# Kernel tuning notes

Measured on AMD Instinct MI355X. Metric: run time of the kernel, lower is better.

The kernel has to match this reference:

```python
import jax, jax.numpy as jnp
import numpy as np

K_MAX_X = 16
K_MAX_T = 16


def _k_actual(N, k_max):
    # low-mode indices [0..k_max] ++ [N-k_max..N-1], mapped to signed frequencies
    idx = np.concatenate([np.arange(k_max + 1), np.arange(N - k_max, N)]).astype(np.float32)
    return np.where(idx <= (N - 1) // 2, idx, idx - N)


def _phase(N, k_max, sign):
    # separable 1D truncated DFT factor: exp(sign*2*pi*i*k*n/N)/sqrt(N), shape [modes, N]
    k = _k_actual(N, k_max)
    n = np.arange(N, dtype=np.float32)
    ang = sign * 2.0 * np.pi * k[:, None] * n[None, :] / N
    return jnp.asarray((np.exp(1j * ang) / np.sqrt(N)).astype(np.complex64))


def setup_inputs() -> dict:
    key = jax.random.key(0)
    k1, k2, k3 = jax.random.split(key, 3)
    B, C_in, C_out, H, W = 16, 64, 64, 128, 128
    modes = 2 * K_MAX_X + 1  # 33
    scale = 1.0 / (C_in * C_out)
    x = jax.random.normal(k1, (B, C_in, H, W), dtype=jnp.float32)
    wr = scale * jax.random.uniform(k2, (C_in, C_out, modes, modes), dtype=jnp.float32)
    wi = scale * jax.random.uniform(k3, (C_in, C_out, modes, modes), dtype=jnp.float32)
    return {"x": x, "weights_real": wr, "weights_imag": wi}


def reference(x, weights_real, weights_imag):
    B, C, H, W = x.shape
    Px_f = _phase(H, K_MAX_X, -1.0)  # [mx, H]
    Pt_f = _phase(W, K_MAX_T, -1.0)  # [mt, W]
    Px_i = _phase(H, K_MAX_X, +1.0)
    Pt_i = _phase(W, K_MAX_T, +1.0)
    xc = x.astype(jnp.complex64)
    # truncated 2D DFT (separable): X[b,c,i,j]
    X = jnp.einsum('bcnm,in,jm->bcij', xc, Px_f, Pt_f)
    R = (weights_real + 1j * weights_imag).astype(jnp.complex64)
    out_kept = jnp.einsum('bcij,coij->boij', X, R)
    # truncated inverse DFT back to grid
    out = jnp.einsum('boij,in,jm->bonm', out_kept, Px_i, Pt_i)
    return jnp.real(out)
```

## Files before the change

kernel.cpp:

```cpp
#include <hip/hip_runtime.h>


#define NB   16
#define NC   64
#define NO   64
#define NH   128
#define NW   128
#define NM   33
#define WMODE (NM*NM)
#define MPAD  1092
#define NIMG 1024

typedef __attribute__((ext_vector_type(8))) short s8v;
typedef __attribute__((ext_vector_type(4))) float f4v;

__device__ inline unsigned short f2bf(float f) {
  union { float f; unsigned u; } v; v.f = f;
  unsigned r = (v.u + 0x7FFFu + ((v.u >> 16) & 1u)) >> 16;
  return (unsigned short)r;
}

__device__ inline s8v pack8(float4 a, float4 b) {
  s8v r;
  r[0] = (short)f2bf(a.x); r[1] = (short)f2bf(a.y);
  r[2] = (short)f2bf(a.z); r[3] = (short)f2bf(a.w);
  r[4] = (short)f2bf(b.x); r[5] = (short)f2bf(b.y);
  r[6] = (short)f2bf(b.z); r[7] = (short)f2bf(b.w);
  return r;
}

__device__ inline uint2 pack4(f4v a) {
  uint2 p;
  p.x = (unsigned)f2bf(a[0]) | ((unsigned)f2bf(a[1]) << 16);
  p.y = (unsigned)f2bf(a[2]) | ((unsigned)f2bf(a[3]) << 16);
  return p;
}

__device__ inline unsigned short phase_bf(int f, int x) {
  if (f >= 66) return 0;
  int g = (f < 33) ? f : f - 33;
  int fr = (g <= 16) ? g : g + 95;
  int ph = (fr * x) & 127;
  float ang = (float)ph * 0.04908738521234052f;
  float v = ((f < 33) ? cosf(ang) : sinf(ang)) * 0.08838834764831845f;
  return f2bf(v);
}

__global__ __launch_bounds__(256) void spc_tables(short* __restrict__ T1,
                                                  short* __restrict__ T2,
                                                  short* __restrict__ T3,
                                                  short* __restrict__ T4) {
  int tid = blockIdx.x * 256 + threadIdx.x;
  if (tid >= 49152) return;
  int f, x; short* dst;
  if (tid < 10240) {
    int e = tid & 7, l = (tid >> 3) & 63, q = tid >> 9;
    int ks = q / 5, jt = q - 5 * ks;
    f = jt * 16 + (l & 15); x = ks * 32 + (l >> 4) * 8 + e; dst = T1 + tid;
  } else if (tid < 20480) {
    int u = tid - 10240;
    int e = u & 7, l = (u >> 3) & 63, q = u >> 9;
    int it = q >> 2, ks = q & 3;
    f = it * 16 + (l & 15); x = ks * 32 + (l >> 4) * 8 + e; dst = T2 + u;
  } else if (tid < 36864) {
    int u = tid - 20480;
    int e = u & 7, l = (u >> 3) & 63, q = u >> 9;
    int cs = q >> 4, ks = (q >> 3) & 1, mt = q & 7;
    int j = ks * 32 + (l >> 4) * 8 + e;
    f = (j < 33) ? cs * 33 + j : 66;
    x = mt * 16 + (l & 15); dst = T3 + u;
  } else {
    int u = tid - 36864;
    int e = u & 7, l = (u >> 3) & 63, q = u >> 9;
    int nt = q / 3, ks = q - 3 * nt;
    int i2 = ks * 32 + (l >> 4) * 8 + e;
    if (i2 < 48) f = (i2 < 33) ? i2 : 66;
    else         f = (i2 - 48 < 33) ? 33 + (i2 - 48) : 66;
    x = nt * 16 + (l & 15); dst = T4 + u;
  }
  *dst = (short)phase_bf(f, x);
}

__global__ __launch_bounds__(256) void spc_fwd_mfma(const float* __restrict__ x,
                                                    const s8v* __restrict__ T1,
                                                    const s8v* __restrict__ T2,
                                                    unsigned* __restrict__ X2u) {
  __shared__ short Wt[80 * 128];
  __shared__ float Gs[80 * 84];
  const int t = threadIdx.x;
  const int l = t & 63;
  const int w = t >> 6;
  const int lr = l & 15;
  const int lg = l >> 4;
  const int img = blockIdx.x;
  const float* xp = x + (size_t)img * (NH * NW);

  for (int nn = 0; nn < 2; ++nn) {
    const int nt = 2 * w + nn;
    const float* xrow = xp + (nt * 16 + lr) * NW + lg * 8;
    s8v a[4];
#pragma unroll
    for (int ks = 0; ks < 4; ++ks) {
      float4 f0 = *reinterpret_cast<const float4*>(xrow + ks * 32);
      float4 f1 = *reinterpret_cast<const float4*>(xrow + ks * 32 + 4);
      a[ks] = pack8(f0, f1);
    }
#pragma unroll
    for (int jt = 0; jt < 5; ++jt) {
      f4v acc = {0.f, 0.f, 0.f, 0.f};
#pragma unroll
      for (int ks = 0; ks < 4; ++ks) {
        s8v b = T1[(ks * 5 + jt) * 64 + l];
        acc = __builtin_amdgcn_mfma_f32_16x16x32_bf16(a[ks], b, acc, 0, 0, 0);
      }
      int j = jt * 16 + lr;
      int g = ((nt * 16 + lg * 4) >> 2) ^ ((j & 7) << 2);
      *reinterpret_cast<uint2*>(&Wt[j * 128 + g * 4]) = pack4(acc);
    }
  }
  __syncthreads();

  for (int tix = w; tix < 25; tix += 4) {
    int it = tix / 5, j2 = tix - 5 * it;
    int jrow = j2 * 16 + lr;
    f4v acc = {0.f, 0.f, 0.f, 0.f};
#pragma unroll
    for (int ks = 0; ks < 4; ++ks) {
      s8v afr = T2[(it * 4 + ks) * 64 + l];
      int g = (ks * 8 + lg * 2) ^ ((jrow & 7) << 2);
      s8v b = *reinterpret_cast<const s8v*>(&Wt[jrow * 128 + g * 4]);
      acc = __builtin_amdgcn_mfma_f32_16x16x32_bf16(afr, b, acc, 0, 0, 0);
    }
    int gi = it * 16 + lg * 4;
#pragma unroll
    for (int r = 0; r < 4; ++r) Gs[(gi + r) * 84 + jrow] = acc[r];
  }
  __syncthreads();

  unsigned* X2p = X2u + (size_t)img * WMODE;
  for (int idx = t; idx < WMODE; idx += 256) {
    int i = idx / 33, j = idx - 33 * i;
    float g11 = Gs[i * 84 + j];
    float g22 = Gs[(i + 33) * 84 + (j + 33)];
    float g12 = Gs[i * 84 + (j + 33)];
    float g21 = Gs[(i + 33) * 84 + j];
    X2p[idx] = (unsigned)f2bf(g11 - g22) | ((unsigned)f2bf(-(g12 + g21)) << 16);
  }
}

__global__ __launch_bounds__(512) void spc_vmix(const float* __restrict__ wr,
                                                const float* __restrict__ wi,
                                                const unsigned* __restrict__ X2u,
                                                short* __restrict__ Kbf) {
  const int t = threadIdx.x;
  const int ml = t & 63;
  const int w = t >> 6;
  const int b0 = w * 2;
  const int o0 = blockIdx.x * 2;
  const int m0 = blockIdx.y * 64;
  const int m = m0 + ml;
  const int mc = (m > 1088) ? 1088 : m;

  const float* wrp = wr + (size_t)o0 * WMODE + mc;
  const float* wip = wi + (size_t)o0 * WMODE + mc;
  const unsigned* xp = X2u + (size_t)(b0 * 64) * WMODE + mc;
  const size_t cstepW = (size_t)64 * WMODE;

  float aR[2][2], aI[2][2];
#pragma unroll
  for (int j = 0; j < 2; ++j)
#pragma unroll
    for (int oo = 0; oo < 2; ++oo) { aR[j][oo] = 0.f; aI[j][oo] = 0.f; }

#pragma unroll 1
  for (int c4 = 0; c4 < 16; ++c4) {
    float wrv[4][2], wiv[4][2];
    unsigned u[4][2];
#pragma unroll
    for (int q = 0; q < 4; ++q) {
      const int c = c4 * 4 + q;
#pragma unroll
      for (int oo = 0; oo < 2; ++oo) {
        wrv[q][oo] = wrp[(size_t)c * cstepW + (size_t)oo * WMODE];
        wiv[q][oo] = wip[(size_t)c * cstepW + (size_t)oo * WMODE];
      }
#pragma unroll
      for (int j = 0; j < 2; ++j)
        u[q][j] = xp[(size_t)(j * 64 + c) * WMODE];
    }
#pragma unroll
    for (int q = 0; q < 4; ++q) {
#pragma unroll
      for (int j = 0; j < 2; ++j) {
        union { unsigned uu; float f; } cv;
        cv.uu = u[q][j] << 16;         const float xr_ = cv.f;
        cv.uu = u[q][j] & 0xFFFF0000u; const float xi_ = cv.f;
#pragma unroll
        for (int oo = 0; oo < 2; ++oo) {
          aR[j][oo] = fmaf(xr_, wrv[q][oo], fmaf(-xi_, wiv[q][oo], aR[j][oo]));
          aI[j][oo] = fmaf(xr_, wiv[q][oo], fmaf( xi_, wrv[q][oo], aI[j][oo]));
        }
      }
    }
  }

  if (m < WMODE) {
#pragma unroll
    for (int j = 0; j < 2; ++j)
#pragma unroll
      for (int oo = 0; oo < 2; ++oo) {
        size_t img = (size_t)(b0 + j) * 64 + o0 + oo;
        Kbf[img * (2 * MPAD) + m]        = (short)f2bf(aR[j][oo]);
        Kbf[img * (2 * MPAD) + MPAD + m] = (short)f2bf(aI[j][oo]);
      }
  }
}

__global__ __launch_bounds__(256) void spc_inv_mfma(const short* __restrict__ Kbf,
                                                    const s8v* __restrict__ T3,
                                                    const s8v* __restrict__ T4,
                                                    float* __restrict__ out) {
  __shared__ short Kls2[2 * MPAD];
  __shared__ short Vt[128 * 128];
  const int t = threadIdx.x;
  const int l = t & 63;
  const int w = t >> 6;
  const int lr = l & 15;
  const int lg = l >> 4;
  const int img = blockIdx.x;

  {
    const uint4* src = reinterpret_cast<const uint4*>(Kbf + (size_t)img * (2 * MPAD));
    uint4* dstl = reinterpret_cast<uint4*>(Kls2);
    for (int idx = t; idx < 273; idx += 256) dstl[idx] = src[idx];
  }
  __syncthreads();

  s8v fr[2][3][2];
#pragma unroll
  for (int ri2 = 0; ri2 < 2; ++ri2)
#pragma unroll
    for (int it = 0; it < 3; ++it)
#pragma unroll
      for (int ks = 0; ks < 2; ++ks) {
        const int i = it * 16 + lr;
#pragma unroll
        for (int e = 0; e < 8; ++e) {
          const int j = ks * 32 + lg * 8 + e;
          unsigned short v = (i < 33 && j < 33)
              ? (unsigned short)Kls2[ri2 * MPAD + i * 33 + j] : (unsigned short)0;
          fr[ri2][it][ks][e] = (short)v;
        }
      }

  for (int mm = 0; mm < 2; ++mm) {
    const int mt = w * 2 + mm;
    const int m = mt * 16 + lr;
    s8v cw[2], sw[2], nsw[2];
#pragma unroll
    for (int ks = 0; ks < 2; ++ks) {
      cw[ks] = T3[((0 * 2 + ks) * 8 + mt) * 64 + l];
      sw[ks] = T3[((1 * 2 + ks) * 8 + mt) * 64 + l];
#pragma unroll
      for (int e = 0; e < 8; ++e)
        nsw[ks][e] = (short)(((unsigned short)sw[ks][e]) ^ 0x8000u);
    }
#pragma unroll
    for (int it = 0; it < 3; ++it) {
      f4v t1 = {0.f, 0.f, 0.f, 0.f}, t2 = {0.f, 0.f, 0.f, 0.f};
#pragma unroll
      for (int ks = 0; ks < 2; ++ks) {
        t1 = __builtin_amdgcn_mfma_f32_16x16x32_bf16(fr[0][it][ks], cw[ks],  t1, 0, 0, 0);
        t1 = __builtin_amdgcn_mfma_f32_16x16x32_bf16(fr[1][it][ks], nsw[ks], t1, 0, 0, 0);
        t2 = __builtin_amdgcn_mfma_f32_16x16x32_bf16(fr[1][it][ks], cw[ks],  t2, 0, 0, 0);
        t2 = __builtin_amdgcn_mfma_f32_16x16x32_bf16(fr[0][it][ks], sw[ks],  t2, 0, 0, 0);
      }
      const int base1 = it * 16 + lg * 4;
      const int g1 = (base1 >> 2) ^ ((m & 7) << 2);
      *reinterpret_cast<uint2*>(&Vt[m * 128 + g1 * 4]) = pack4(t1);
      f4v nt2v = {-t2[0], -t2[1], -t2[2], -t2[3]};
      const int g2 = ((48 + base1) >> 2) ^ ((m & 7) << 2);
      *reinterpret_cast<uint2*>(&Vt[m * 128 + g2 * 4]) = pack4(nt2v);
    }
  }
  __syncthreads();

  float* op = out + (size_t)img * (NH * NW);
  for (int nn = 0; nn < 2; ++nn) {
    const int nt = w * 2 + nn;
    s8v a[3];
#pragma unroll
    for (int ks = 0; ks < 3; ++ks) a[ks] = T4[(nt * 3 + ks) * 64 + l];
    for (int mt = 0; mt < 8; ++mt) {
      const int m = mt * 16 + lr;
      f4v acc = {0.f, 0.f, 0.f, 0.f};
#pragma unroll
      for (int ks = 0; ks < 3; ++ks) {
        const int g = (ks * 8 + lg * 2) ^ ((m & 7) << 2);
        s8v bb = *reinterpret_cast<const s8v*>(&Vt[m * 128 + g * 4]);
        acc = __builtin_amdgcn_mfma_f32_16x16x32_bf16(a[ks], bb, acc, 0, 0, 0);
      }
      const int n = nt * 16 + lg * 4;
#pragma unroll
      for (int r = 0; r < 4; ++r) op[(n + r) * NW + m] = acc[r];
    }
  }
}

extern "C" void kernel_launch(void* const* d_in, const int* in_sizes, int n_in,
                              void* d_out, int out_size, void* d_ws, size_t ws_size,
                              hipStream_t stream) {
  const float* x  = (const float*)d_in[0];
  const float* wr = (const float*)d_in[1];
  const float* wi = (const float*)d_in[2];
  float* out = (float*)d_out;

  char* ws = (char*)d_ws;
  short* T1 = (short*)(ws);
  short* T2 = (short*)(ws + 20480);
  short* T3 = (short*)(ws + 40960);
  short* T4 = (short*)(ws + 73728);
  unsigned* X2u = (unsigned*)(ws + 98304);
  short* Kbf = (short*)(ws + 4558848);

  hipLaunchKernelGGL(spc_tables, dim3(192), dim3(256), 0, stream, T1, T2, T3, T4);
  hipLaunchKernelGGL(spc_fwd_mfma, dim3(NIMG), dim3(256), 0, stream,
                     x, (const s8v*)T1, (const s8v*)T2, X2u);
  hipLaunchKernelGGL(spc_vmix, dim3(32, 18), dim3(512), 0, stream,
                     wr, wi, X2u, Kbf);
  hipLaunchKernelGGL(spc_inv_mfma, dim3(NIMG), dim3(256), 0, stream,
                     Kbf, (const s8v*)T3, (const s8v*)T4, out);
}
```

Baseline: 76.56 us.

## Share vmix weight loads across waves via LDS with double-buffered async prefetch

In the channel-mixing kernel, all eight waves of a block previously loaded the same real and imaginary weight values from global memory. Now each wave fetches two of the sixteen weight rows per channel group straight into a double-buffered LDS tile with global_load_lds. The next group's X values are prefetched into registers while the current group is computed. This cuts redundant global weight traffic and overlaps loads with FMAs, at the cost of two block barriers per iteration and a dependence on correct wait-count handling for the async LDS loads.

After: 72.23 us. -5.7%, faster.

```diff
diff --git a/kernel.cpp b/kernel.cpp
--- a/kernel.cpp
+++ b/kernel.cpp
@@ -34,6 +34,12 @@
   p.x = (unsigned)f2bf(a[0]) | ((unsigned)f2bf(a[1]) << 16);
   p.y = (unsigned)f2bf(a[2]) | ((unsigned)f2bf(a[3]) << 16);
   return p;
+}
+
+__device__ inline void gload_lds4(const float* g, float* lds) {
+  auto* gp = (const __attribute__((address_space(1))) unsigned*)(uintptr_t)g;
+  auto* lp = (__attribute__((address_space(3))) unsigned*)(uintptr_t)lds;
+  __builtin_amdgcn_global_load_lds(gp, lp, 4, 0, 0);
 }
 
 __device__ inline unsigned short phase_bf(int f, int x) {
@@ -152,6 +158,7 @@
                                                 const float* __restrict__ wi,
                                                 const unsigned* __restrict__ X2u,
                                                 short* __restrict__ Kbf) {
+  __shared__ float Lw[2][16 * 64];
   const int t = threadIdx.x;
   const int ml = t & 63;
   const int w = t >> 6;
@@ -161,10 +168,18 @@
   const int m = m0 + ml;
   const int mc = (m > 1088) ? 1088 : m;
 
-  const float* wrp = wr + (size_t)o0 * WMODE + mc;
-  const float* wip = wi + (size_t)o0 * WMODE + mc;
   const unsigned* xp = X2u + (size_t)(b0 * 64) * WMODE + mc;
-  const size_t cstepW = (size_t)64 * WMODE;
+
+  const int g0 = w * 2;
+  const int q_[2]  = {g0 >> 2, (g0 + 1) >> 2};
+  const int oo_[2] = {(g0 >> 1) & 1, ((g0 + 1) >> 1) & 1};
+  const int pl_[2] = {g0 & 1, (g0 + 1) & 1};
+  const float* wsrc[2];
+#pragma unroll
+  for (int gi = 0; gi < 2; ++gi)
+    wsrc[gi] = (pl_[gi] ? wi : wr) +
+               (size_t)((q_[gi] * 64 + o0 + oo_[gi])) * WMODE + mc;
+  const size_t wCstep = (size_t)4 * 64 * WMODE;
 
   float aR[2][2], aI[2][2];
 #pragma unroll
@@ -172,33 +187,78 @@
 #pragma unroll
     for (int oo = 0; oo < 2; ++oo) { aR[j][oo] = 0.f; aI[j][oo] = 0.f; }
 
+  unsigned uA[4][2], uB[4][2];
+
+#pragma unroll
+  for (int gi = 0; gi < 2; ++gi)
+    gload_lds4(wsrc[gi], &Lw[0][(g0 + gi) * 64]);
+#pragma unroll
+  for (int q = 0; q < 4; ++q)
+#pragma unroll
+    for (int j = 0; j < 2; ++j)
+      uA[q][j] = xp[(size_t)(j * 64 + q) * WMODE];
+
 #pragma unroll 1
-  for (int c4 = 0; c4 < 16; ++c4) {
-    float wrv[4][2], wiv[4][2];
-    unsigned u[4][2];
+  for (int k = 0; k < 16; k += 2) {
+    __syncthreads();
+    if (k + 1 < 16) {
+#pragma unroll
+      for (int gi = 0; gi < 2; ++gi)
+        gload_lds4(wsrc[gi] + (size_t)(k + 1) * wCstep, &Lw[1][(g0 + gi) * 64]);
+#pragma unroll
+      for (int q = 0; q < 4; ++q)
+#pragma unroll
+        for (int j = 0; j < 2; ++j)
+          uB[q][j] = xp[(size_t)(j * 64 + (k + 1) * 4 + q) * WMODE];
+    }
 #pragma unroll
     for (int q = 0; q < 4; ++q) {
-      const int c = c4 * 4 + q;
+      float wrv[2], wiv[2];
 #pragma unroll
       for (int oo = 0; oo < 2; ++oo) {
-        wrv[q][oo] = wrp[(size_t)c * cstepW + (size_t)oo * WMODE];
-        wiv[q][oo] = wip[(size_t)c * cstepW + (size_t)oo * WMODE];
-      }
-#pragma unroll
-      for (int j = 0; j < 2; ++j)
-        u[q][j] = xp[(size_t)(j * 64 + c) * WMODE];
-    }
-#pragma unroll
-    for (int q = 0; q < 4; ++q) {
+        wrv[oo] = Lw[0][(q * 4 + oo * 2 + 0) * 64 + ml];
+        wiv[oo] = Lw[0][(q * 4 + oo * 2 + 1) * 64 + ml];
+      }
 #pragma unroll
       for (int j = 0; j < 2; ++j) {
         union { unsigned uu; float f; } cv;
-        cv.uu = u[q][j] << 16;         const float xr_ = cv.f;
-        cv.uu = u[q][j] & 0xFFFF0000u; const float xi_ = cv.f;
+        cv.uu = uA[q][j] << 16;         const float xr_ = cv.f;
+        cv.uu = uA[q][j] & 0xFFFF0000u; const float xi_ = cv.f;
 #pragma unroll
         for (int oo = 0; oo < 2; ++oo) {
-          aR[j][oo] = fmaf(xr_, wrv[q][oo], fmaf(-xi_, wiv[q][oo], aR[j][oo]));
-          aI[j][oo] = fmaf(xr_, wiv[q][oo], fmaf( xi_, wrv[q][oo], aI[j][oo]));
+          aR[j][oo] = fmaf(xr_, wrv[oo], fmaf(-xi_, wiv[oo], aR[j][oo]));
+          aI[j][oo] = fmaf(xr_, wiv[oo], fmaf( xi_, wrv[oo], aI[j][oo]));
+        }
+      }
+    }
+    __syncthreads();
+    if (k + 2 < 16) {
+#pragma unroll
+      for (int gi = 0; gi < 2; ++gi)
+        gload_lds4(wsrc[gi] + (size_t)(k + 2) * wCstep, &Lw[0][(g0 + gi) * 64]);
+#pragma unroll
+      for (int q = 0; q < 4; ++q)
+#pragma unroll
+        for (int j = 0; j < 2; ++j)
+          uA[q][j] = xp[(size_t)(j * 64 + (k + 2) * 4 + q) * WMODE];
+    }
+#pragma unroll
+    for (int q = 0; q < 4; ++q) {
+      float wrv[2], wiv[2];
+#pragma unroll
+      for (int oo = 0; oo < 2; ++oo) {
+        wrv[oo] = Lw[1][(q * 4 + oo * 2 + 0) * 64 + ml];
+        wiv[oo] = Lw[1][(q * 4 + oo * 2 + 1) * 64 + ml];
+      }
+#pragma unroll
+      for (int j = 0; j < 2; ++j) {
+        union { unsigned uu; float f; } cv;
+        cv.uu = uB[q][j] << 16;         const float xr_ = cv.f;
+        cv.uu = uB[q][j] & 0xFFFF0000u; const float xi_ = cv.f;
+#pragma unroll
+        for (int oo = 0; oo < 2; ++oo) {
+          aR[j][oo] = fmaf(xr_, wrv[oo], fmaf(-xi_, wiv[oo], aR[j][oo]));
+          aI[j][oo] = fmaf(xr_, wiv[oo], fmaf( xi_, wrv[oo], aI[j][oo]));
         }
       }
     }
```

## Prepack mixing weights to bf16 complex and stream vmix operands via LDS

Applied to the files above, without the earlier changes.

Adds a kernel that converts the fp32 real and imaginary weights into packed bf16 complex words, laid out as [o][mode chunk][c][64] so vmix reads contiguous blocks. The vmix kernel now loads weights and spectral coefficients with global_load_lds into a double-buffered shared-memory pipeline, using explicit waitcnt to overlap loads with the FMAs. This halves the weight bytes vmix reads and hides load latency, at the cost of an extra pack pass over the weights on every call and lower weight precision.

After: 83.35 us. 8.9% more time.

```diff
diff --git a/kernel.cpp b/kernel.cpp
--- a/kernel.cpp
+++ b/kernel.cpp
@@ -20,6 +20,13 @@
   return (unsigned short)r;
 }
 
+__device__ inline float bflo(unsigned u) {
+  union { unsigned u; float f; } cv; cv.u = u << 16; return cv.f;
+}
+__device__ inline float bfhi(unsigned u) {
+  union { unsigned u; float f; } cv; cv.u = u & 0xFFFF0000u; return cv.f;
+}
+
 __device__ inline s8v pack8(float4 a, float4 b) {
   s8v r;
   r[0] = (short)f2bf(a.x); r[1] = (short)f2bf(a.y);
@@ -34,6 +41,12 @@
   p.x = (unsigned)f2bf(a[0]) | ((unsigned)f2bf(a[1]) << 16);
   p.y = (unsigned)f2bf(a[2]) | ((unsigned)f2bf(a[3]) << 16);
   return p;
+}
+
+__device__ inline void gload_lds4(const void* g, void* lds) {
+  auto* gp = (const __attribute__((address_space(1))) unsigned*)(uintptr_t)g;
+  auto* lp = (__attribute__((address_space(3))) unsigned*)(uintptr_t)lds;
+  __builtin_amdgcn_global_load_lds(gp, lp, 4, 0, 0);
 }
 
 __device__ inline unsigned short phase_bf(int f, int x) {
@@ -81,6 +94,57 @@
   *dst = (short)phase_bf(f, x);
 }
 
+__global__ __launch_bounds__(256) void spc_wpack(const float* __restrict__ wr,
+                                                 const float* __restrict__ wi,
+                                                 unsigned* __restrict__ Wp) {
+  __shared__ float Lf[4][2][8][64];
+  const int t = threadIdx.x;
+  const int ml = t & 63;
+  const int w = t >> 6;
+  const int oct = blockIdx.x;
+  const int c = blockIdx.y;
+
+  auto src_of = [&](int task, const float* base) -> const float* {
+    int o_loc = task / 18, chunk = task - 18 * o_loc;
+    int o = oct * 8 + o_loc;
+    int m = chunk * 64 + ml; if (m > 1088) m = 1088;
+    return base + (size_t)(c * 64 + o) * WMODE + m;
+  };
+  auto issue = [&](int k, int buf) {
+#pragma unroll
+    for (int q = 0; q < 4; ++q) {
+      int task = w * 36 + k * 4 + q;
+      gload_lds4(src_of(task, wr), &Lf[w][buf][q * 2 + 0][0]);
+      gload_lds4(src_of(task, wi), &Lf[w][buf][q * 2 + 1][0]);
+    }
+  };
+
+  issue(0, 0);
+  issue(1, 1);
+#pragma unroll 1
+  for (int k = 0; k < 9; ++k) {
+    if (k < 8) asm volatile("s_waitcnt vmcnt(8)" ::: "memory");
+    else       asm volatile("s_waitcnt vmcnt(0)" ::: "memory");
+    const int buf = k & 1;
+    float av[4], bv[4];
+#pragma unroll
+    for (int q = 0; q < 4; ++q) {
+      av[q] = Lf[w][buf][q * 2 + 0][ml];
+      bv[q] = Lf[w][buf][q * 2 + 1][ml];
+    }
+    asm volatile("s_waitcnt lgkmcnt(0)" ::: "memory");
+    if (k + 2 < 9) issue(k + 2, buf);
+#pragma unroll
+    for (int q = 0; q < 4; ++q) {
+      int task = w * 36 + k * 4 + q;
+      int o_loc = task / 18, chunk = task - 18 * o_loc;
+      int o = oct * 8 + o_loc;
+      unsigned u = (unsigned)f2bf(av[q]) | ((unsigned)f2bf(bv[q]) << 16);
+      Wp[(((size_t)o * 18 + chunk) * 64 + c) * 64 + ml] = u;
+    }
+  }
+}
+
 __global__ __launch_bounds__(256) void spc_fwd_mfma(const float* __restrict__ x,
                                                     const s8v* __restrict__ T1,
                                                     const s8v* __restrict__ T2,
@@ -148,23 +212,34 @@
   }
 }
 
-__global__ __launch_bounds__(512) void spc_vmix(const float* __restrict__ wr,
-                                                const float* __restrict__ wi,
+__global__ __launch_bounds__(512) void spc_vmix(const unsigned* __restrict__ Wp,
                                                 const unsigned* __restrict__ X2u,
                                                 short* __restrict__ Kbf) {
+  __shared__ unsigned Lv[8][2][16][64];
   const int t = threadIdx.x;
   const int ml = t & 63;
   const int w = t >> 6;
   const int b0 = w * 2;
   const int o0 = blockIdx.x * 2;
-  const int m0 = blockIdx.y * 64;
-  const int m = m0 + ml;
-  const int mc = (m > 1088) ? 1088 : m;
-
-  const float* wrp = wr + (size_t)o0 * WMODE + mc;
-  const float* wip = wi + (size_t)o0 * WMODE + mc;
-  const unsigned* xp = X2u + (size_t)(b0 * 64) * WMODE + mc;
-  const size_t cstepW = (size_t)64 * WMODE;
+  const int chunk = blockIdx.y;
+  const int m = chunk * 64 + ml;
+  const int mcl = (m > 1088) ? 1088 : m;
+
+  const unsigned* wb0 = Wp + (((size_t)o0 * 18 + chunk) * 64) * 64 + ml;
+  const unsigned* wb1 = Wp + ((((size_t)o0 + 1) * 18 + chunk) * 64) * 64 + ml;
+  const unsigned* xb0 = X2u + (size_t)((b0 + 0) * 64) * WMODE + mcl;
+  const unsigned* xb1 = X2u + (size_t)((b0 + 1) * 64) * WMODE + mcl;
+
+  auto issue = [&](int k, int buf) {
+#pragma unroll
+    for (int q = 0; q < 4; ++q) {
+      const int cc = k * 4 + q;
+      gload_lds4(wb0 + (size_t)cc * 64, &Lv[w][buf][q * 2 + 0][0]);
+      gload_lds4(wb1 + (size_t)cc * 64, &Lv[w][buf][q * 2 + 1][0]);
+      gload_lds4(xb0 + (size_t)cc * WMODE, &Lv[w][buf][8 + q * 2 + 0][0]);
+      gload_lds4(xb1 + (size_t)cc * WMODE, &Lv[w][buf][8 + q * 2 + 1][0]);
+    }
+  };
 
   float aR[2][2], aI[2][2];
 #pragma unroll
@@ -172,35 +247,35 @@
 #pragma unroll
     for (int oo = 0; oo < 2; ++oo) { aR[j][oo] = 0.f; aI[j][oo] = 0.f; }
 
+  issue(0, 0);
+  issue(1, 1);
 #pragma unroll 1
-  for (int c4 = 0; c4 < 16; ++c4) {
-    float wrv[4][2], wiv[4][2];
-    unsigned u[4][2];
+  for (int k = 0; k < 16; ++k) {
+    if (k < 15) asm volatile("s_waitcnt vmcnt(16)" ::: "memory");
+    else        asm volatile("s_waitcnt vmcnt(0)" ::: "memory");
+    const int buf = k & 1;
+    unsigned wv[8], xv[8];
+#pragma unroll
+    for (int g = 0; g < 8; ++g) {
+      wv[g] = Lv[w][buf][g][ml];
+      xv[g] = Lv[w][buf][8 + g][ml];
+    }
+    asm volatile("s_waitcnt lgkmcnt(0)" ::: "memory");
+    if (k + 2 < 16) issue(k + 2, buf);
 #pragma unroll
     for (int q = 0; q < 4; ++q) {
-      const int c = c4 * 4 + q;
-#pragma unroll
-      for (int oo = 0; oo < 2; ++oo) {
-        wrv[q][oo] = wrp[(size_t)c * cstepW + (size_t)oo * WMODE];
-        wiv[q][oo] = wip[(size_t)c * cstepW + (size_t)oo * WMODE];
-      }
-#pragma unroll
-      for (int j = 0; j < 2; ++j)
-        u[q][j] = xp[(size_t)(j * 64 + c) * WMODE];
-    }
-#pragma unroll
-    for (int q = 0; q < 4; ++q) {
-#pragma unroll
-      for (int j = 0; j < 2; ++j) {
-        union { unsigned uu; float f; } cv;
-        cv.uu = u[q][j] << 16;         const float xr_ = cv.f;
-        cv.uu = u[q][j] & 0xFFFF0000u; const float xi_ = cv.f;
-#pragma unroll
-        for (int oo = 0; oo < 2; ++oo) {
-          aR[j][oo] = fmaf(xr_, wrv[q][oo], fmaf(-xi_, wiv[q][oo], aR[j][oo]));
-          aI[j][oo] = fmaf(xr_, wiv[q][oo], fmaf( xi_, wrv[q][oo], aI[j][oo]));
-        }
-      }
+      const float wr0 = bflo(wv[q * 2 + 0]), wi0 = bfhi(wv[q * 2 + 0]);
+      const float wr1 = bflo(wv[q * 2 + 1]), wi1 = bfhi(wv[q * 2 + 1]);
+      const float x0r = bflo(xv[q * 2 + 0]), x0i = bfhi(xv[q * 2 + 0]);
+      const float x1r = bflo(xv[q * 2 + 1]), x1i = bfhi(xv[q * 2 + 1]);
+      aR[0][0] = fmaf(x0r, wr0, fmaf(-x0i, wi0, aR[0][0]));
+      aI[0][0] = fmaf(x0r, wi0, fmaf( x0i, wr0, aI[0][0]));
+      aR[0][1] = fmaf(x0r, wr1, fmaf(-x0i, wi1, aR[0][1]));
+      aI[0][1] = fmaf(x0r, wi1, fmaf( x0i, wr1, aI[0][1]));
+      aR[1][0] = fmaf(x1r, wr0, fmaf(-x1i, wi0, aR[1][0]));
+      aI[1][0] = fmaf(x1r, wi0, fmaf( x1i, wr0, aI[1][0]));
+      aR[1][1] = fmaf(x1r, wr1, fmaf(-x1i, wi1, aR[1][1]));
+      aI[1][1] = fmaf(x1r, wi1, fmaf( x1i, wr1, aI[1][1]));
     }
   }
 
@@ -322,12 +397,14 @@
   short* T4 = (short*)(ws + 73728);
   unsigned* X2u = (unsigned*)(ws + 98304);
   short* Kbf = (short*)(ws + 4558848);
+  unsigned* Wp = (unsigned*)(ws + 9031680);
 
   hipLaunchKernelGGL(spc_tables, dim3(192), dim3(256), 0, stream, T1, T2, T3, T4);
+  hipLaunchKernelGGL(spc_wpack, dim3(8, 64), dim3(256), 0, stream, wr, wi, Wp);
   hipLaunchKernelGGL(spc_fwd_mfma, dim3(NIMG), dim3(256), 0, stream,
                      x, (const s8v*)T1, (const s8v*)T2, X2u);
   hipLaunchKernelGGL(spc_vmix, dim3(32, 18), dim3(512), 0, stream,
-                     wr, wi, X2u, Kbf);
+                     Wp, X2u, Kbf);
   hipLaunchKernelGGL(spc_inv_mfma, dim3(NIMG), dim3(256), 0, stream,
                      Kbf, (const s8v*)T3, (const s8v*)T4, out);
 }
```

## Split channel reduction in vmix across two blocks and sum partials in inverse

Applied to the files above, without the earlier changes.

Splits the mode-mixing kernel's input-channel reduction into two halves via a third grid dimension, which doubles the number of blocks (576 to 1152) and gives the GPU more parallelism. Each half writes fp32 partial sums to a workspace. The inverse kernel then loads both partials, adds them and converts to bf16 while staging into LDS. The cost is roughly four times more intermediate traffic (two fp32 buffers instead of one bf16 buffer) and extra loads in the inverse kernel.

After: 72.11 us. -5.8%, faster.

```diff
diff --git a/kernel.cpp b/kernel.cpp
--- a/kernel.cpp
+++ b/kernel.cpp
@@ -18,6 +18,13 @@
   union { float f; unsigned u; } v; v.f = f;
   unsigned r = (v.u + 0x7FFFu + ((v.u >> 16) & 1u)) >> 16;
   return (unsigned short)r;
+}
+
+__device__ inline float bflo(unsigned u) {
+  union { unsigned u; float f; } cv; cv.u = u << 16; return cv.f;
+}
+__device__ inline float bfhi(unsigned u) {
+  union { unsigned u; float f; } cv; cv.u = u & 0xFFFF0000u; return cv.f;
 }
 
 __device__ inline s8v pack8(float4 a, float4 b) {
@@ -151,19 +158,21 @@
 __global__ __launch_bounds__(512) void spc_vmix(const float* __restrict__ wr,
                                                 const float* __restrict__ wi,
                                                 const unsigned* __restrict__ X2u,
-                                                short* __restrict__ Kbf) {
+                                                float* __restrict__ Kp) {
   const int t = threadIdx.x;
   const int ml = t & 63;
   const int w = t >> 6;
   const int b0 = w * 2;
   const int o0 = blockIdx.x * 2;
   const int m0 = blockIdx.y * 64;
+  const int ch = blockIdx.z;
+  const int c_base = ch * 32;
   const int m = m0 + ml;
   const int mc = (m > 1088) ? 1088 : m;
 
-  const float* wrp = wr + (size_t)o0 * WMODE + mc;
-  const float* wip = wi + (size_t)o0 * WMODE + mc;
-  const unsigned* xp = X2u + (size_t)(b0 * 64) * WMODE + mc;
+  const float* wrp = wr + (size_t)(c_base * 64 + o0) * WMODE + mc;
+  const float* wip = wi + (size_t)(c_base * 64 + o0) * WMODE + mc;
+  const unsigned* xp = X2u + (size_t)(b0 * 64 + c_base) * WMODE + mc;
   const size_t cstepW = (size_t)64 * WMODE;
 
   float aR[2][2], aI[2][2];
@@ -173,7 +182,7 @@
     for (int oo = 0; oo < 2; ++oo) { aR[j][oo] = 0.f; aI[j][oo] = 0.f; }
 
 #pragma unroll 1
-  for (int c4 = 0; c4 < 16; ++c4) {
+  for (int c4 = 0; c4 < 8; ++c4) {
     float wrv[4][2], wiv[4][2];
     unsigned u[4][2];
 #pragma unroll
@@ -192,9 +201,8 @@
     for (int q = 0; q < 4; ++q) {
 #pragma unroll
       for (int j = 0; j < 2; ++j) {
-        union { unsigned uu; float f; } cv;
-        cv.uu = u[q][j] << 16;         const float xr_ = cv.f;
-        cv.uu = u[q][j] & 0xFFFF0000u; const float xi_ = cv.f;
+        const float xr_ = bflo(u[q][j]);
+        const float xi_ = bfhi(u[q][j]);
 #pragma unroll
         for (int oo = 0; oo < 2; ++oo) {
           aR[j][oo] = fmaf(xr_, wrv[q][oo], fmaf(-xi_, wiv[q][oo], aR[j][oo]));
@@ -210,13 +218,14 @@
 #pragma unroll
       for (int oo = 0; oo < 2; ++oo) {
         size_t img = (size_t)(b0 + j) * 64 + o0 + oo;
-        Kbf[img * (2 * MPAD) + m]        = (short)f2bf(aR[j][oo]);
-        Kbf[img * (2 * MPAD) + MPAD + m] = (short)f2bf(aI[j][oo]);
-      }
-  }
-}
-
-__global__ __launch_bounds__(256) void spc_inv_mfma(const short* __restrict__ Kbf,
+        float* dst = Kp + ((size_t)ch * NIMG + img) * (2 * MPAD);
+        dst[m]        = aR[j][oo];
+        dst[MPAD + m] = aI[j][oo];
+      }
+  }
+}
+
+__global__ __launch_bounds__(256) void spc_inv_mfma(const float* __restrict__ Kp,
                                                     const s8v* __restrict__ T3,
                                                     const s8v* __restrict__ T4,
                                                     float* __restrict__ out) {
@@ -230,9 +239,18 @@
   const int img = blockIdx.x;
 
   {
-    const uint4* src = reinterpret_cast<const uint4*>(Kbf + (size_t)img * (2 * MPAD));
-    uint4* dstl = reinterpret_cast<uint4*>(Kls2);
-    for (int idx = t; idx < 273; idx += 256) dstl[idx] = src[idx];
+    const float4* p0 = reinterpret_cast<const float4*>(
+        Kp + ((size_t)0 * NIMG + img) * (2 * MPAD));
+    const float4* p1 = reinterpret_cast<const float4*>(
+        Kp + ((size_t)1 * NIMG + img) * (2 * MPAD));
+    for (int idx = t; idx < 546; idx += 256) {
+      float4 a = p0[idx];
+      float4 b = p1[idx];
+      uint2 u;
+      u.x = (unsigned)f2bf(a.x + b.x) | ((unsigned)f2bf(a.y + b.y) << 16);
+      u.y = (unsigned)f2bf(a.z + b.z) | ((unsigned)f2bf(a.w + b.w) << 16);
+      *reinterpret_cast<uint2*>(&Kls2[idx * 4]) = u;
+    }
   }
   __syncthreads();
 
@@ -321,13 +339,13 @@
   short* T3 = (short*)(ws + 40960);
   short* T4 = (short*)(ws + 73728);
   unsigned* X2u = (unsigned*)(ws + 98304);
-  short* Kbf = (short*)(ws + 4558848);
+  float* Kp = (float*)(ws + 4558848);
 
   hipLaunchKernelGGL(spc_tables, dim3(192), dim3(256), 0, stream, T1, T2, T3, T4);
   hipLaunchKernelGGL(spc_fwd_mfma, dim3(NIMG), dim3(256), 0, stream,
                      x, (const s8v*)T1, (const s8v*)T2, X2u);
-  hipLaunchKernelGGL(spc_vmix, dim3(32, 18), dim3(512), 0, stream,
-                     wr, wi, X2u, Kbf);
+  hipLaunchKernelGGL(spc_vmix, dim3(32, 18, 2), dim3(512), 0, stream,
+                     wr, wi, X2u, Kp);
   hipLaunchKernelGGL(spc_inv_mfma, dim3(NIMG), dim3(256), 0, stream,
-                     Kbf, (const s8v*)T3, (const s8v*)T4, out);
-}
+                     Kp, (const s8v*)T3, (const s8v*)T4, out);
+}
```
